# Kernel tuning notes

Hardware: AMD Instinct MI355X
Metric: run time of the kernel (lower is better)

## Reference

```python
import jax, jax.numpy as jnp
import numpy as np

B, LE, LD = 8, 4096, 4096
DE, DD, A = 512, 512, 128


def setup_inputs() -> dict:
    key = jax.random.key(0)
    ks = jax.random.split(key, 9)
    f32 = jnp.float32
    return {
        "encoder_outputs": jax.random.normal(ks[0], (B, LE, DE), f32),
        "decoder_outputs": jax.random.normal(ks[1], (B, LD, DD), f32),
        # linear_q / linear_k / linear_v (Dense with bias, relu activation)
        "Wq": jax.random.normal(ks[2], (DD, A), f32) * 0.05,
        "bq": jnp.zeros((A,), f32),
        "Wk": jax.random.normal(ks[3], (DE, A), f32) * 0.05,
        "bk": jnp.zeros((A,), f32),
        "Wv": jax.random.normal(ks[4], (DE, A), f32) * 0.05,
        "bv": jnp.zeros((A,), f32),
        # perceptron branch weights (Dense, no bias)
        "Pw": jax.random.normal(ks[5], (A, A), f32) * 0.05,
        "Pu": jax.random.normal(ks[6], (A, A), f32) * 0.05,
        "pv": jax.random.normal(ks[7], (A, 1), f32) * 0.05,
    }


def reference(encoder_outputs, decoder_outputs, Wq, bq, Wk, bk, Wv, bv, Pw, Pu, pv):
    att = Wq.shape[1]
    q = jax.nn.relu(decoder_outputs @ Wq + bq)   # [B, Ld, A]
    k = jax.nn.relu(encoder_outputs @ Wk + bk)   # [B, Le, A]
    v = jax.nn.relu(encoder_outputs @ Wv + bv)   # [B, Le, A]
    # perceptron score: pv^T (Pw q_i + Pu k_j). No nonlinearity between the
    # sum and pv, so it decomposes additively -> no [B,Ld,Le,A] tiling needed.
    q_term = (q @ Pw) @ pv                        # [B, Ld, 1]
    k_term = (k @ Pu) @ pv                        # [B, Le, 1]
    scores = (q_term + jnp.swapaxes(k_term, 1, 2)) / jnp.sqrt(jnp.float32(att))  # [B, Ld, Le]
    weights = jax.nn.softmax(scores, axis=-1)
    attention = jnp.einsum('bij,bjd->bid', weights, v)  # [B, Ld, A]
    return attention
```

## Files before the change

### kernel.cpp

```cpp
#include <hip/hip_runtime.h>
#include <hip/hip_bf16.h>

#define B_   8
#define KDIM 512
#define AA_  128
#define RTOT 32768
#define BM   32
#define NGRID (RTOT/BM)

typedef __attribute__((ext_vector_type(8))) short short8;
typedef __attribute__((ext_vector_type(4))) float f32x4;

#define WCT_OFF   0
#define U_OFF     262144
#define BIAS_OFF  262656
#define PARTS_OFF 263680
#define S_OFF     296448
#define VB_OFF    427520

__device__ inline ushort f2bf(float f) {
    union { float f; unsigned u; } x; x.f = f;
    unsigned r = x.u + 0x7fffu + ((x.u >> 16) & 1u);
    return (ushort)(r >> 16);
}
__device__ inline float bf2f(ushort s) {
    union { unsigned u; float f; } x; x.u = ((unsigned)s) << 16;
    return x.f;
}

__device__ __forceinline__ void glds16(const void* g, void* l) {
    __builtin_amdgcn_global_load_lds(
        (const __attribute__((address_space(1))) void*)g,
        (__attribute__((address_space(3))) void*)l, 16, 0, 0);
}

__global__ void prep_kernel(const float* __restrict__ Wk, const float* __restrict__ bk,
                            const float* __restrict__ Wv, const float* __restrict__ bv,
                            const float* __restrict__ Pu, const float* __restrict__ pv,
                            ushort* __restrict__ wct, float* __restrict__ u,
                            float* __restrict__ bias) {
    int t = threadIdx.x;
    int base = blockIdx.x * 256 + t;
    for (int i = 0; i < 4; ++i) {
        int idx = base + i * 32768;
        int n = idx >> 9, k = idx & 511;
        float s = (n < 128) ? Wk[k * 128 + n] : Wv[k * 128 + (n - 128)];
        wct[idx] = f2bf(s);
    }
    if (blockIdx.x == 0) {
        if (t < 128) {
            float acc = 0.f;
            for (int c = 0; c < 128; ++c) acc += Pu[t * 128 + c] * pv[c];
            u[t] = acc;
        }
        bias[t] = (t < 128) ? bk[t] : bv[t - 128];
    }
}

__global__ __launch_bounds__(256, 4)
void gemm_fused(const float* __restrict__ enc, const ushort* __restrict__ wct,
                const float* __restrict__ bias, const float* __restrict__ u,
                ushort* __restrict__ vbuf, float* __restrict__ sout) {
    __shared__ ushort As[BM][72];
    __shared__ ushort Bs[256][64];
    __shared__ float s_red[BM][2];
    const int t = threadIdx.x;
    const int wv = t >> 6, l = t & 63;
    const int m = l & 15, kb = l >> 4;
    const int rg = kb;
    const int row0 = blockIdx.x * BM;

    const int ar = t >> 3, ak8 = (t & 7) * 8;
    const float* aptr = enc + (size_t)(row0 + ar) * KDIM + ak8;

    const int brow = (l >> 3);
    const int bcolB = (l & 7) << 4;

    f32x4 acc[2][4] = {};
    float4 a0, a1;

    a0 = *(const float4*)aptr;
    a1 = *(const float4*)(aptr + 4);

    for (int st = 0; st < 8; ++st) {
        {
            const char* gbase = (const char*)wct + (size_t)st * 128 + bcolB;
#pragma unroll
            for (int i = 0; i < 8; ++i) {
                int c = (wv << 3) | i;
                int row = (c << 3) + brow;
                glds16(gbase + (size_t)row * 1024,
                       (char*)Bs + c * 1024 + l * 16);
            }
            int4 pk;
            pk.x = (int)f2bf(a0.x) | ((int)f2bf(a0.y) << 16);
            pk.y = (int)f2bf(a0.z) | ((int)f2bf(a0.w) << 16);
            pk.z = (int)f2bf(a1.x) | ((int)f2bf(a1.y) << 16);
            pk.w = (int)f2bf(a1.z) | ((int)f2bf(a1.w) << 16);
            *(int4*)&As[ar][ak8] = pk;
        }
        __syncthreads();
        if (st < 7) {
            const float* ap = aptr + (st + 1) * 64;
            a0 = *(const float4*)ap;
            a1 = *(const float4*)(ap + 4);
        }
#pragma unroll
        for (int kc = 0; kc < 2; ++kc) {
            short8 afr[2], bfr[4];
#pragma unroll
            for (int mt = 0; mt < 2; ++mt)
                afr[mt] = *(const short8*)&As[mt * 16 + m][kc * 32 + kb * 8];
#pragma unroll
            for (int nt = 0; nt < 4; ++nt)
                bfr[nt] = *(const short8*)&Bs[wv * 64 + nt * 16 + m][kc * 32 + kb * 8];
#pragma unroll
            for (int mt = 0; mt < 2; ++mt)
#pragma unroll
                for (int nt = 0; nt < 4; ++nt)
                    acc[mt][nt] = __builtin_amdgcn_mfma_f32_16x16x32_bf16(
                        afr[mt], bfr[nt], acc[mt][nt], 0, 0, 0);
        }
        __syncthreads();
    }

    if (wv < 2) {
#pragma unroll
        for (int mt = 0; mt < 2; ++mt) {
            float p[4] = {0.f, 0.f, 0.f, 0.f};
#pragma unroll
            for (int nt = 0; nt < 4; ++nt) {
                int col = wv * 64 + nt * 16 + m;
                float bsv = bias[col], uw = u[col];
#pragma unroll
                for (int j = 0; j < 4; ++j) {
                    float vvv = acc[mt][nt][j] + bsv;
                    vvv = vvv > 0.f ? vvv : 0.f;
                    p[j] += vvv * uw;
                }
            }
#pragma unroll
            for (int j = 0; j < 4; ++j) {
                p[j] += __shfl_xor(p[j], 1);
                p[j] += __shfl_xor(p[j], 2);
                p[j] += __shfl_xor(p[j], 4);
                p[j] += __shfl_xor(p[j], 8);
            }
            if (m == 0) {
#pragma unroll
                for (int j = 0; j < 4; ++j)
                    s_red[mt * 16 + rg * 4 + j][wv] = p[j];
            }
        }
    } else {
#pragma unroll
        for (int mt = 0; mt < 2; ++mt) {
#pragma unroll
            for (int nt = 0; nt < 4; ++nt) {
                int col = wv * 64 + nt * 16 + m;
                float bsv = bias[col];
#pragma unroll
                for (int j = 0; j < 4; ++j) {
                    int rowl = mt * 16 + rg * 4 + j;
                    float vvv = acc[mt][nt][j] + bsv;
                    vvv = vvv > 0.f ? vvv : 0.f;
                    vbuf[(size_t)(row0 + rowl) * AA_ + (col - 128)] = f2bf(vvv);
                }
            }
        }
    }
    __syncthreads();
    if (t < BM) sout[row0 + t] = s_red[t][0] + s_red[t][1];
}

__global__ __launch_bounds__(256)
void wsum_kernel(const ushort* __restrict__ vbuf, const float* __restrict__ sg,
                 float* __restrict__ parts) {
    __shared__ float redM[5], redS[5];
    __shared__ float pw[4][128];
    const int blk = blockIdx.x;
    const int b = blk >> 3, ch = blk & 7;
    const int t = threadIdx.x, wv = t >> 6, l = t & 63;
    const float inv_s = 0.08838834764831843f;

    float vl[16], mx = -1e30f;
#pragma unroll
    for (int i = 0; i < 16; ++i) {
        vl[i] = sg[b * 4096 + i * 256 + t];
        mx = fmaxf(mx, vl[i]);
    }
#pragma unroll
    for (int off = 1; off < 64; off <<= 1) mx = fmaxf(mx, __shfl_xor(mx, off));
    if (l == 0) redM[wv] = mx;
    __syncthreads();
    if (t == 0) redM[4] = fmaxf(fmaxf(redM[0], redM[1]), fmaxf(redM[2], redM[3]));
    __syncthreads();
    const float M = redM[4];
    float sm = 0.f;
#pragma unroll
    for (int i = 0; i < 16; ++i) sm += __expf((vl[i] - M) * inv_s);
#pragma unroll
    for (int off = 1; off < 64; off <<= 1) sm += __shfl_xor(sm, off);
    if (l == 0) redS[wv] = sm;
    __syncthreads();
    if (t == 0) redS[4] = 1.0f / (redS[0] + redS[1] + redS[2] + redS[3]);
    __syncthreads();
    const float rS = redS[4];

    const int rg = l >> 4, d8 = (l & 15) * 8;
    const int rbase = b * 4096 + ch * 512;
    float acc[8] = {};
    for (int it = 0; it < 32; ++it) {
        int r = rbase + it * 16 + wv * 4 + rg;
        float wj = __expf((sg[r] - M) * inv_s) * rS;
        short8 vvv = *(const short8*)(vbuf + (size_t)r * AA_ + d8);
#pragma unroll
        for (int j = 0; j < 8; ++j)
            acc[j] += wj * bf2f((ushort)vvv[j]);
    }
#pragma unroll
    for (int j = 0; j < 8; ++j) {
        acc[j] += __shfl_xor(acc[j], 16);
        acc[j] += __shfl_xor(acc[j], 32);
    }
    if (l < 16) {
#pragma unroll
        for (int j = 0; j < 8; ++j) pw[wv][d8 + j] = acc[j];
    }
    __syncthreads();
    if (t < 128) parts[blk * 128 + t] = pw[0][t] + pw[1][t] + pw[2][t] + pw[3][t];
}

__global__ __launch_bounds__(256)
void bcast_kernel(const float* __restrict__ parts, float4* __restrict__ out) {
    __shared__ float4 nv[32];
    const int t = threadIdx.x;
    const int c = blockIdx.x * 256 + t;
    const int b = (blockIdx.x * 1024) >> 19;
    if (t < 32) {
        const float4* p4 = (const float4*)parts;
        float4 s = {0.f, 0.f, 0.f, 0.f};
#pragma unroll
        for (int ch = 0; ch < 8; ++ch) {
            float4 q = p4[(b * 8 + ch) * 32 + t];
            s.x += q.x; s.y += q.y; s.z += q.z; s.w += q.w;
        }
        nv[t] = s;
    }
    __syncthreads();
    out[c] = nv[t & 31];
}

extern "C" void kernel_launch(void* const* d_in, const int* in_sizes, int n_in,
                              void* d_out, int out_size, void* d_ws, size_t ws_size,
                              hipStream_t stream) {
    const float* enc = (const float*)d_in[0];
    const float* Wk = (const float*)d_in[4];
    const float* bk = (const float*)d_in[5];
    const float* Wv = (const float*)d_in[6];
    const float* bv = (const float*)d_in[7];
    const float* Pu = (const float*)d_in[9];
    const float* pv = (const float*)d_in[10];

    char* ws = (char*)d_ws;
    ushort* wct   = (ushort*)(ws + WCT_OFF);
    float*  u     = (float*)(ws + U_OFF);
    float*  bias  = (float*)(ws + BIAS_OFF);
    float*  parts = (float*)(ws + PARTS_OFF);
    float*  sg    = (float*)(ws + S_OFF);
    ushort* vbuf  = (ushort*)(ws + VB_OFF);

    prep_kernel<<<128, 256, 0, stream>>>(Wk, bk, Wv, bv, Pu, pv, wct, u, bias);
    gemm_fused<<<NGRID, 256, 0, stream>>>(enc, wct, bias, u, vbuf, sg);
    wsum_kernel<<<64, 256, 0, stream>>>(vbuf, sg, parts);
    bcast_kernel<<<4096, 256, 0, stream>>>(parts, (float4*)d_out);
}
```

Measured before the change: 181.4 us.

## Double-buffer GEMM weight tiles with swizzle, larger row tile, rebalance reduction kernels

Doubles the GEMM row tile to 64 rows per block and double-buffers the bf16 weight tiles in LDS, prefetching the next K-stage with async global-to-LDS loads under manual waitcnt and barriers. It also XOR-swizzles the weight layout in prep to cut LDS bank conflicts. The weighted-sum kernel is split into 4x more blocks for parallelism, and the broadcast kernel uses fewer blocks that each write more output. Risks include lower occupancy from the larger LDS and register footprint, and correctness that depends on the hand-written vmcnt counts.

```diff
diff --git a/kernel.cpp b/kernel.cpp
--- a/kernel.cpp
+++ b/kernel.cpp
@@ -5,7 +5,7 @@
 #define KDIM 512
 #define AA_  128
 #define RTOT 32768
-#define BM   32
+#define BM   64
 #define NGRID (RTOT/BM)
 
 typedef __attribute__((ext_vector_type(8))) short short8;
@@ -15,8 +15,8 @@
 #define U_OFF     262144
 #define BIAS_OFF  262656
 #define PARTS_OFF 263680
-#define S_OFF     296448
-#define VB_OFF    427520
+#define S_OFF     394752
+#define VB_OFF    525824
 
 __device__ inline ushort f2bf(float f) {
     union { float f; unsigned u; } x; x.f = f;
@@ -43,9 +43,12 @@
     int base = blockIdx.x * 256 + t;
     for (int i = 0; i < 4; ++i) {
         int idx = base + i * 32768;
-        int n = idx >> 9, k = idx & 511;
-        float s = (n < 128) ? Wk[k * 128 + n] : Wv[k * 128 + (n - 128)];
-        wct[idx] = f2bf(s);
+        int n = idx >> 9, kdst = idx & 511;
+        int st = kdst >> 6, s = (kdst >> 3) & 7, e = kdst & 7;
+        int j = s ^ (n & 7);
+        int ksrc = st * 64 + j * 8 + e;
+        float v = (n < 128) ? Wk[ksrc * 128 + n] : Wv[ksrc * 128 + (n - 128)];
+        wct[idx] = f2bf(v);
     }
     if (blockIdx.x == 0) {
         if (t < 128) {
@@ -57,76 +60,99 @@
     }
 }
 
-__global__ __launch_bounds__(256, 4)
+__global__ __launch_bounds__(256, 2)
 void gemm_fused(const float* __restrict__ enc, const ushort* __restrict__ wct,
                 const float* __restrict__ bias, const float* __restrict__ u,
                 ushort* __restrict__ vbuf, float* __restrict__ sout) {
+    __shared__ ushort Bs[2][256 * 64];
     __shared__ ushort As[BM][72];
-    __shared__ ushort Bs[256][64];
     __shared__ float s_red[BM][2];
     const int t = threadIdx.x;
     const int wv = t >> 6, l = t & 63;
     const int m = l & 15, kb = l >> 4;
-    const int rg = kb;
     const int row0 = blockIdx.x * BM;
 
-    const int ar = t >> 3, ak8 = (t & 7) * 8;
-    const float* aptr = enc + (size_t)(row0 + ar) * KDIM + ak8;
-
-    const int brow = (l >> 3);
-    const int bcolB = (l & 7) << 4;
-
-    f32x4 acc[2][4] = {};
-    float4 a0, a1;
-
-    a0 = *(const float4*)aptr;
-    a1 = *(const float4*)(aptr + 4);
-
+    const int ar0 = t >> 3, ak8 = (t & 7) * 8;
+    const float* ap0 = enc + (size_t)(row0 + ar0) * KDIM + ak8;
+    const float* ap1 = ap0 + (size_t)32 * KDIM;
+
+    const char* wct_c = (const char*)wct;
+
+    f32x4 acc[4][4] = {};
+    float4 a0, a1, a2, a3;
+
+    a0 = *(const float4*)ap0; a1 = *(const float4*)(ap0 + 4);
+    a2 = *(const float4*)ap1; a3 = *(const float4*)(ap1 + 4);
+#pragma unroll
+    for (int i = 0; i < 8; ++i) {
+        int c = (wv << 3) | i;
+        int row = (c << 3) + (l >> 3);
+        glds16(wct_c + (size_t)row * 1024 + ((l & 7) << 4),
+               (char*)&Bs[0][0] + c * 1024 + l * 16);
+    }
+
+#pragma unroll
     for (int st = 0; st < 8; ++st) {
+        const int bufc = st & 1;
         {
-            const char* gbase = (const char*)wct + (size_t)st * 128 + bcolB;
-#pragma unroll
-            for (int i = 0; i < 8; ++i) {
-                int c = (wv << 3) | i;
-                int row = (c << 3) + brow;
-                glds16(gbase + (size_t)row * 1024,
-                       (char*)Bs + c * 1024 + l * 16);
-            }
             int4 pk;
             pk.x = (int)f2bf(a0.x) | ((int)f2bf(a0.y) << 16);
             pk.y = (int)f2bf(a0.z) | ((int)f2bf(a0.w) << 16);
             pk.z = (int)f2bf(a1.x) | ((int)f2bf(a1.y) << 16);
             pk.w = (int)f2bf(a1.z) | ((int)f2bf(a1.w) << 16);
-            *(int4*)&As[ar][ak8] = pk;
-        }
-        __syncthreads();
+            *(int4*)&As[ar0][ak8] = pk;
+            pk.x = (int)f2bf(a2.x) | ((int)f2bf(a2.y) << 16);
+            pk.y = (int)f2bf(a2.z) | ((int)f2bf(a2.w) << 16);
+            pk.z = (int)f2bf(a3.x) | ((int)f2bf(a3.y) << 16);
+            pk.w = (int)f2bf(a3.z) | ((int)f2bf(a3.w) << 16);
+            *(int4*)&As[ar0 + 32][ak8] = pk;
+        }
         if (st < 7) {
-            const float* ap = aptr + (st + 1) * 64;
-            a0 = *(const float4*)ap;
-            a1 = *(const float4*)(ap + 4);
-        }
+            const float* p0 = ap0 + (st + 1) * 64;
+            const float* p1 = ap1 + (st + 1) * 64;
+            a0 = *(const float4*)p0; a1 = *(const float4*)(p0 + 4);
+            a2 = *(const float4*)p1; a3 = *(const float4*)(p1 + 4);
+            const char* gb = wct_c + (size_t)(st + 1) * 128;
+#pragma unroll
+            for (int i = 0; i < 8; ++i) {
+                int c = (wv << 3) | i;
+                int row = (c << 3) + (l >> 3);
+                glds16(gb + (size_t)row * 1024 + ((l & 7) << 4),
+                       (char*)&Bs[bufc ^ 1][0] + c * 1024 + l * 16);
+            }
+            asm volatile("s_waitcnt vmcnt(12) lgkmcnt(0)" ::: "memory");
+        } else {
+            asm volatile("s_waitcnt vmcnt(0) lgkmcnt(0)" ::: "memory");
+        }
+        __builtin_amdgcn_sched_barrier(0);
+        __builtin_amdgcn_s_barrier();
 #pragma unroll
         for (int kc = 0; kc < 2; ++kc) {
-            short8 afr[2], bfr[4];
-#pragma unroll
-            for (int mt = 0; mt < 2; ++mt)
+            short8 afr[4], bfr[4];
+#pragma unroll
+            for (int mt = 0; mt < 4; ++mt)
                 afr[mt] = *(const short8*)&As[mt * 16 + m][kc * 32 + kb * 8];
 #pragma unroll
-            for (int nt = 0; nt < 4; ++nt)
-                bfr[nt] = *(const short8*)&Bs[wv * 64 + nt * 16 + m][kc * 32 + kb * 8];
-#pragma unroll
-            for (int mt = 0; mt < 2; ++mt)
+            for (int nt = 0; nt < 4; ++nt) {
+                int r = wv * 64 + nt * 16 + m;
+                int s = (kc * 4 + kb) ^ (r & 7);
+                bfr[nt] = *(const short8*)&Bs[bufc][r * 64 + s * 8];
+            }
+#pragma unroll
+            for (int mt = 0; mt < 4; ++mt)
 #pragma unroll
                 for (int nt = 0; nt < 4; ++nt)
                     acc[mt][nt] = __builtin_amdgcn_mfma_f32_16x16x32_bf16(
                         afr[mt], bfr[nt], acc[mt][nt], 0, 0, 0);
         }
-        __syncthreads();
-    }
-
+        asm volatile("" ::: "memory");
+        __builtin_amdgcn_s_barrier();
+    }
+
+    const int rg = kb;
     if (wv < 2) {
 #pragma unroll
-        for (int mt = 0; mt < 2; ++mt) {
+        for (int mt = 0; mt < 4; ++mt) {
             float p[4] = {0.f, 0.f, 0.f, 0.f};
 #pragma unroll
             for (int nt = 0; nt < 4; ++nt) {
@@ -154,7 +180,7 @@
         }
     } else {
 #pragma unroll
-        for (int mt = 0; mt < 2; ++mt) {
+        for (int mt = 0; mt < 4; ++mt) {
 #pragma unroll
             for (int nt = 0; nt < 4; ++nt) {
                 int col = wv * 64 + nt * 16 + m;
@@ -179,7 +205,7 @@
     __shared__ float redM[5], redS[5];
     __shared__ float pw[4][128];
     const int blk = blockIdx.x;
-    const int b = blk >> 3, ch = blk & 7;
+    const int b = blk >> 5, ch = blk & 31;
     const int t = threadIdx.x, wv = t >> 6, l = t & 63;
     const float inv_s = 0.08838834764831843f;
 
@@ -208,9 +234,10 @@
     const float rS = redS[4];
 
     const int rg = l >> 4, d8 = (l & 15) * 8;
-    const int rbase = b * 4096 + ch * 512;
+    const int rbase = b * 4096 + ch * 128;
     float acc[8] = {};
-    for (int it = 0; it < 32; ++it) {
+#pragma unroll
+    for (int it = 0; it < 8; ++it) {
         int r = rbase + it * 16 + wv * 4 + rg;
         float wj = __expf((sg[r] - M) * inv_s) * rS;
         short8 vvv = *(const short8*)(vbuf + (size_t)r * AA_ + d8);
@@ -233,22 +260,24 @@
 
 __global__ __launch_bounds__(256)
 void bcast_kernel(const float* __restrict__ parts, float4* __restrict__ out) {
-    __shared__ float4 nv[32];
+    __shared__ float redp[2][128];
+    __shared__ float nvf[128];
     const int t = threadIdx.x;
-    const int c = blockIdx.x * 256 + t;
-    const int b = (blockIdx.x * 1024) >> 19;
-    if (t < 32) {
-        const float4* p4 = (const float4*)parts;
-        float4 s = {0.f, 0.f, 0.f, 0.f};
-#pragma unroll
-        for (int ch = 0; ch < 8; ++ch) {
-            float4 q = p4[(b * 8 + ch) * 32 + t];
-            s.x += q.x; s.y += q.y; s.z += q.z; s.w += q.w;
-        }
-        nv[t] = s;
-    }
-    __syncthreads();
-    out[c] = nv[t & 31];
+    const int b = blockIdx.x >> 7;
+    const int d = t & 127, h = t >> 7;
+    float s = 0.f;
+#pragma unroll
+    for (int i = 0; i < 16; ++i)
+        s += parts[(size_t)(b * 32 + h * 16 + i) * 128 + d];
+    redp[h][d] = s;
+    __syncthreads();
+    if (t < 128) nvf[t] = redp[0][t] + redp[1][t];
+    __syncthreads();
+    const float4 val = ((const float4*)nvf)[t & 31];
+    float4* o4 = out + (size_t)blockIdx.x * 1024;
+#pragma unroll
+    for (int it = 0; it < 4; ++it)
+        o4[it * 256 + t] = val;
 }
 
 extern "C" void kernel_launch(void* const* d_in, const int* in_sizes, int n_in,
@@ -272,6 +301,6 @@
 
     prep_kernel<<<128, 256, 0, stream>>>(Wk, bk, Wv, bv, Pu, pv, wct, u, bias);
     gemm_fused<<<NGRID, 256, 0, stream>>>(enc, wct, bias, u, vbuf, sg);
-    wsum_kernel<<<64, 256, 0, stream>>>(vbuf, sg, parts);
-    bcast_kernel<<<4096, 256, 0, stream>>>(parts, (float4*)d_out);
-}
+    wsum_kernel<<<256, 256, 0, stream>>>(vbuf, sg, parts);
+    bcast_kernel<<<1024, 256, 0, stream>>>(parts, (float4*)d_out);
+}
```

Result: faster. 177.3 us (-2.3%).
